# Performance work log

Hardware: AMD Instinct MI355X
Metric: run time of the kernel (lower is better)

## Reference

```python
import jax, jax.numpy as jnp
import numpy as np

MARGIN = 0.3
N = 8192
D = 128
NUM_CLASSES = 256

def setup_inputs() -> dict:
    key = jax.random.key(0)
    k1, k2 = jax.random.split(key)
    inputs = jax.random.normal(k1, (N, D), dtype=jnp.float32)
    targets = jax.random.randint(k2, (N,), 0, NUM_CLASSES, dtype=jnp.int64)
    return {"inputs": inputs, "targets": targets}

def reference(inputs, targets):
    n = inputs.shape[0]
    dt = inputs.dtype
    # pairwise euclidean distances: ||xi||^2 + ||xj||^2 - 2 xi.xj, clamped and sqrt'ed
    sq = jnp.sum(inputs * inputs, axis=1)                     # [n]
    d2 = sq[:, None] + sq[None, :] - 2.0 * (inputs @ inputs.T)
    dist = jnp.sqrt(jnp.clip(d2, 1e-12, None))                # [n, n]
    dsq = dist * dist                                         # squared dists used by the loss

    mask = targets[:, None] == targets[None, :]               # same-identity mask [n, n]

    # positives: torch code sorts and drops the smallest (the self-distance ~1e-6)
    pos_d = jnp.where(mask, dist, jnp.inf)
    min_idx = jnp.argmin(pos_d, axis=1)                       # index of dropped element per row
    excl = jnp.arange(n)[None, :] == min_idx[:, None]
    pos_valid = mask & ~excl                                  # remaining positives
    cnt_p = jnp.sum(pos_valid, axis=1).astype(dt)
    sigma_p = jnp.sum(jnp.where(pos_valid, dsq, 0.0), axis=1) / cnt_p
    max_p = jnp.max(jnp.where(pos_valid, dsq, -jnp.inf), axis=1)
    dist_ap = max_p / sigma_p + 0.5 * jnp.log(sigma_p)        # [n]

    # negatives: all different-identity entries
    neg = ~mask
    cnt_n = jnp.sum(neg, axis=1).astype(dt)
    sigma_n = jnp.sum(jnp.where(neg, dsq, 0.0), axis=1) / cnt_n
    min_n = jnp.min(jnp.where(neg, dsq, jnp.inf), axis=1)
    dist_an = min_n / sigma_n + 0.5 * jnp.log(sigma_n)        # [n]

    # MarginRankingLoss with y=1: mean(max(0, -(an - ap) + margin))
    loss = jnp.mean(jnp.maximum(dist_ap - dist_an + MARGIN, 0.0))
    return loss
```

## Files before the change

kernel.cpp:

```cpp
#include <hip/hip_runtime.h>
#include <math.h>


#define NROWS 8192
#define MARGIN_F 0.3f

typedef short bf16x8 __attribute__((ext_vector_type(8)));
typedef float f32x16 __attribute__((ext_vector_type(16)));
union U4B { uint4 u; bf16x8 h; };

__device__ __forceinline__ unsigned short f2bf(float x) {
    unsigned u = __float_as_uint(x);
    return (unsigned short)((u + 0x7fffu + ((u >> 16) & 1u)) >> 16);
}
__device__ __forceinline__ float bflo(unsigned u) { return __uint_as_float(u << 16); }
__device__ __forceinline__ float bfhi(unsigned u) { return __uint_as_float(u & 0xffff0000u); }

__global__ __launch_bounds__(256) void prep_kernel(const float* __restrict__ X,
                                                   const int* __restrict__ tgt,
                                                   float* __restrict__ sq,
                                                   float* __restrict__ upk,
                                                   unsigned int* __restrict__ Xbf,
                                                   unsigned int* __restrict__ Xbfn,
                                                   int* __restrict__ hist,
                                                   int* __restrict__ ccnt,
                                                   int* __restrict__ cstart,
                                                   float* __restrict__ S_class,
                                                   float* __restrict__ bsum,
                                                   float* __restrict__ rowsum) {
    __shared__ int h[256];
    __shared__ int csh[256];
    __shared__ int wsum[4];
    __shared__ float rsm[4][128];
    __shared__ float bs[4];
    int tid = threadIdx.x, w = tid >> 6, l = tid & 63;
    int bx = blockIdx.x;

    h[tid] = 0;
    __syncthreads();
    const int4* t4 = (const int4*)tgt;
    for (int i = tid; i < NROWS / 4; i += 256) {
        int4 v = t4[i];
        atomicAdd(&h[v.x], 1);
        atomicAdd(&h[v.y], 1);
        atomicAdd(&h[v.z], 1);
        atomicAdd(&h[v.w], 1);
    }
    __syncthreads();
    int hv = h[tid];
    int x = hv;
    #pragma unroll
    for (int d = 1; d < 64; d <<= 1) {
        int y = __shfl_up(x, d, 64);
        if ((tid & 63) >= d) x += y;
    }
    if ((tid & 63) == 63) wsum[tid >> 6] = x;
    __syncthreads();
    int off = 0;
    for (int i = 0; i < (tid >> 6); ++i) off += wsum[i];
    int excl = off + x - hv;
    csh[tid] = excl;
    if (bx == 0) {
        hist[tid] = hv;
        cstart[tid] = excl;
        if (tid == 255) cstart[256] = NROWS;
    }

    int row0 = bx * 32 + w * 8;
    unsigned h2s[8];
    float s8[8];
    int c8[8];
    float rsx = 0.0f, rsy = 0.0f, rs = 0.0f;
    #pragma unroll
    for (int i = 0; i < 8; ++i) {
        int r = row0 + i;
        float2 v = ((const float2*)X)[(size_t)r * 64 + l];
        unsigned hx = f2bf(v.x), hy = f2bf(v.y);
        h2s[i] = hx | (hy << 16);
        rsx += v.x; rsy += v.y;
        float s = v.x * v.x + v.y * v.y;
        for (int d = 32; d > 0; d >>= 1) s += __shfl_down(s, d, 64);
        if (l == 0) {
            c8[i] = tgt[r];
            s8[i] = s;
            rs += s;
        }
    }
    rsm[w][2 * l] = rsx;
    rsm[w][2 * l + 1] = rsy;
    if (l == 0) bs[w] = rs;
    __syncthreads();
    if (tid < 128)
        atomicAdd(&rowsum[tid], rsm[0][tid] + rsm[1][tid] + rsm[2][tid] + rsm[3][tid]);
    if (tid == 0) bsum[bx] = bs[0] + bs[1] + bs[2] + bs[3];

    #pragma unroll
    for (int i = 0; i < 8; ++i) {
        int pos = 0;
        if (l == 0) {
            int c = c8[i];
            pos = csh[c] + atomicAdd(&ccnt[c], 1);
            sq[pos] = s8[i];
            upk[pos] = __uint_as_float((__float_as_uint(0.5f * s8[i]) & 0xffffff00u) | (unsigned)c);
            atomicAdd(&S_class[c], s8[i]);
        }
        pos = __shfl(pos, 0, 64);
        int g = pos >> 5, rr = pos & 31;
        size_t idx = ((size_t)(g * 16 + (l >> 2)) * 32 + rr) * 4 + (l & 3);
        unsigned hh = h2s[i];
        Xbf[idx] = hh;
        Xbfn[idx] = hh ^ 0x80008000u;
    }
}

__global__ __launch_bounds__(256, 3) void dist_kernel(
        const unsigned short* __restrict__ Xbf, const unsigned short* __restrict__ Xbfn,
        const float* __restrict__ upk, const int* __restrict__ cstart,
        float4* __restrict__ partial, int ns_mask, int jb_shift, int tiles) {
    __shared__ float4 sm[64 * 4];
    const int tid = threadIdx.x;
    const int w = tid >> 6, l = tid & 63, hl = l >> 5, l31 = l & 31;
    const int bx = blockIdx.x;
    const int slice = bx & ns_mask;
    const int jb = bx >> jb_shift;
    const int col0 = jb * 64;
    const uint4* Xq = (const uint4*)Xbf;
    const uint4* Xqn = (const uint4*)Xbfn;

    bf16x8 Bf[2][8];
    #pragma unroll
    for (int ct = 0; ct < 2; ++ct) {
        const uint4* bp = Xq + (size_t)(jb * 2 + ct) * 512 + hl * 32 + l31;
        #pragma unroll
        for (int kk = 0; kk < 8; ++kk) {
            U4B tb; tb.u = bp[kk * 64];
            Bf[ct][kk] = tb.h;
        }
    }
    int tjt[2];
    tjt[0] = __float_as_int(upk[col0 + l31]) & 0xff;
    tjt[1] = __float_as_int(upk[col0 + 32 + l31]) & 0xff;
    const int c_first = __float_as_int(upk[col0]) & 0xff;
    const int c_last  = __float_as_int(upk[col0 + 63]) & 0xff;
    const int U0 = cstart[c_first];
    const int U1 = cstart[c_last + 1];

    float Ss[2] = {0.f, 0.f};
    float Mp[2] = {-INFINITY, -INFINITY};
    float Mn[2] = { INFINITY,  INFINITY};
    const int row_base = slice * tiles * 128;

    for (int t = 0; t < tiles; ++t) {
        const int i0 = row_base + t * 128;

        float ur[16];
        const float4* up = (const float4*)(upk + i0 + w * 32 + 4 * hl);
        #pragma unroll
        for (int g = 0; g < 4; ++g) {
            float4 u4 = up[g * 2];
            ur[g * 4 + 0] = u4.x; ur[g * 4 + 1] = u4.y;
            ur[g * 4 + 2] = u4.z; ur[g * 4 + 3] = u4.w;
        }

        f32x16 ainit;
        #pragma unroll
        for (int r = 0; r < 16; ++r) ainit[r] = ur[r];
        f32x16 acc[2];
        acc[0] = ainit;
        acc[1] = ainit;
        const uint4* ap = Xqn + ((size_t)(i0 >> 5) + w) * 512 + hl * 32 + l31;
        #pragma unroll
        for (int kk = 0; kk < 8; ++kk) {
            U4B a; a.u = ap[kk * 64];
            acc[0] = __builtin_amdgcn_mfma_f32_32x32x16_bf16(a.h, Bf[0][kk], acc[0], 0, 0, 0);
            acc[1] = __builtin_amdgcn_mfma_f32_32x32x16_bf16(a.h, Bf[1][kk], acc[1], 0, 0, 0);
        }

        if (i0 < U1 && i0 + 128 > U0) {
            #pragma unroll
            for (int ct = 0; ct < 2; ++ct) {
                const int tt = tjt[ct];
                #pragma unroll
                for (int r = 0; r < 16; ++r) {
                    float v = acc[ct][r];
                    bool same = ((__float_as_int(ur[r]) & 0xff) == tt);
                    float a = ur[r] - v;
                    Ss[ct] += same ? a : 0.0f;
                    Mp[ct] = fmaxf(Mp[ct], same ? v : -INFINITY);
                    Mn[ct] = same ? Mn[ct] : fminf(Mn[ct], v);
                }
            }
        } else {
            #pragma unroll
            for (int ct = 0; ct < 2; ++ct) {
                #pragma unroll
                for (int r = 0; r < 16; r += 2)
                    Mn[ct] = fminf(fminf(acc[ct][r], acc[ct][r + 1]), Mn[ct]);
            }
        }
    }

    #pragma unroll
    for (int ct = 0; ct < 2; ++ct) {
        Ss[ct] += __shfl_xor(Ss[ct], 32, 64);
        Mp[ct] = fmaxf(Mp[ct], __shfl_xor(Mp[ct], 32, 64));
        Mn[ct] = fminf(Mn[ct], __shfl_xor(Mn[ct], 32, 64));
    }
    if (l < 32) {
        #pragma unroll
        for (int ct = 0; ct < 2; ++ct)
            sm[(ct * 32 + l31) * 4 + w] = make_float4(Ss[ct], Mp[ct], Mn[ct], 0.0f);
    }
    __syncthreads();
    if (tid < 64) {
        float4 a = sm[tid * 4 + 0], b = sm[tid * 4 + 1];
        float4 c2 = sm[tid * 4 + 2], d = sm[tid * 4 + 3];
        float4 o;
        o.x = a.x + b.x + c2.x + d.x;
        o.y = fmaxf(fmaxf(a.y, b.y), fmaxf(c2.y, d.y));
        o.z = fminf(fminf(a.z, b.z), fminf(c2.z, d.z));
        o.w = 0.0f;
        partial[(size_t)slice * NROWS + col0 + tid] = o;
    }
}

__global__ __launch_bounds__(256) void combine_kernel(
        const float* __restrict__ sq, const float* __restrict__ upk,
        const unsigned int* __restrict__ Xbf,
        const int* __restrict__ hist, const float* __restrict__ S_class,
        const float* __restrict__ bsum, const float* __restrict__ rowsum,
        const float4* __restrict__ partial,
        float* __restrict__ blocksum, int* __restrict__ done,
        float* __restrict__ out, int ns) {
    __shared__ float red[4];
    __shared__ float hs[4];
    __shared__ float rsl[128];
    __shared__ int lastflag;
    int tid = threadIdx.x, l = tid & 63, w = tid >> 6;

    if (tid < 128) rsl[tid] = rowsum[tid];

    float b = bsum[tid];
    for (int d = 32; d > 0; d >>= 1) b += __shfl_down(b, d, 64);
    if (l == 0) red[w] = b;
    __syncthreads();
    float S_all = red[0] + red[1] + red[2] + red[3];

    int j = blockIdx.x * 256 + tid;
    float Ss = 0.f, Mp = -INFINITY, Mn = INFINITY;
    for (int s = 0; s < ns; ++s) {
        float4 p = partial[(size_t)s * NROWS + j];
        Ss += p.x;
        Mp = fmaxf(Mp, p.y); Mn = fminf(Mn, p.z);
    }

    float sa = 0.0f;
    {
        const uint4* Xq = (const uint4*)Xbf;
        int g = j >> 5, rr = j & 31;
        #pragma unroll
        for (int c16 = 0; c16 < 16; ++c16) {
            uint4 q = Xq[((size_t)(g * 16 + c16)) * 32 + rr];
            int k0 = c16 * 8;
            sa = fmaf(bflo(q.x), rsl[k0 + 0], sa);
            sa = fmaf(bfhi(q.x), rsl[k0 + 1], sa);
            sa = fmaf(bflo(q.y), rsl[k0 + 2], sa);
            sa = fmaf(bfhi(q.y), rsl[k0 + 3], sa);
            sa = fmaf(bflo(q.z), rsl[k0 + 4], sa);
            sa = fmaf(bfhi(q.z), rsl[k0 + 5], sa);
            sa = fmaf(bflo(q.w), rsl[k0 + 6], sa);
            sa = fmaf(bfhi(q.w), rsl[k0 + 7], sa);
        }
    }

    float sqj = sq[j];
    int c = __float_as_int(upk[j]) & 0xff;
    float cnt = (float)hist[c];
    float sumall = (float)NROWS * sqj + S_all - 2.0f * sa;
    float sump = cnt * sqj + S_class[c] - 2.0f * Ss;
    float sumn = sumall - sump;
    float sigp = sump / (cnt - 1.0f);
    float sign_ = sumn / ((float)NROWS - cnt);
    float ap = (sqj + 2.0f * Mp) / sigp + 0.5f * __logf(sigp);
    float an = (sqj + 2.0f * Mn) / sign_ + 0.5f * __logf(sign_);
    float h = fmaxf(ap - an + MARGIN_F, 0.0f);
    for (int d = 32; d > 0; d >>= 1) h += __shfl_down(h, d, 64);
    if (l == 0) hs[w] = h;
    __syncthreads();
    if (tid == 0) {
        float tot = hs[0] + hs[1] + hs[2] + hs[3];
        __hip_atomic_store(&blocksum[blockIdx.x], tot,
                           __ATOMIC_RELEASE, __HIP_MEMORY_SCOPE_AGENT);
        int prev = __hip_atomic_fetch_add(done, 1,
                                          __ATOMIC_ACQ_REL, __HIP_MEMORY_SCOPE_AGENT);
        lastflag = (prev == 31) ? 1 : 0;
    }
    __syncthreads();
    if (lastflag) {
        float s2 = 0.0f;
        if (tid < 32)
            s2 = __hip_atomic_load(&blocksum[tid],
                                   __ATOMIC_ACQUIRE, __HIP_MEMORY_SCOPE_AGENT);
        if (tid < 64) {
            for (int d = 32; d > 0; d >>= 1) s2 += __shfl_down(s2, d, 64);
            if (tid == 0) out[0] = s2 * (1.0f / NROWS);
        }
    }
}

extern "C" void kernel_launch(void* const* d_in, const int* in_sizes, int n_in,
                              void* d_out, int out_size, void* d_ws, size_t ws_size,
                              hipStream_t stream) {
    const float* X = (const float*)d_in[0];
    const int* tgt = (const int*)d_in[1];
    float* out = (float*)d_out;

    float* f = (float*)d_ws;
    int*   hist     = (int*)f;
    float* S_class  = f + 256;
    int*   ccnt     = (int*)(f + 512);
    float* rowsum   = f + 768;
    int*   done     = (int*)(f + 897);
    float* bsum     = f + 1024;
    float* blocksum = f + 1280;
    int*   cstart   = (int*)(f + 1536);
    float* sq       = f + 2048;
    float* upk      = f + 10240;
    unsigned int* Xbf  = (unsigned int*)(f + 18432);
    unsigned int* Xbfn = (unsigned int*)(f + 542720);
    float4* partial = (float4*)(f + 1067008);

    int ns = 8;
    while (ns > 2 && ws_size < ((size_t)1067008 + (size_t)ns * NROWS * 4) * sizeof(float))
        ns >>= 1;
    int shift = (ns == 8) ? 3 : (ns == 4) ? 2 : 1;
    int tiles = 64 / ns;

    hipMemsetAsync(d_ws, 0, 3600, stream);
    prep_kernel<<<256, 256, 0, stream>>>(X, tgt, sq, upk, Xbf, Xbfn,
                                         hist, ccnt, cstart, S_class, bsum, rowsum);
    dist_kernel<<<128 * ns, 256, 0, stream>>>((const unsigned short*)Xbf,
                                              (const unsigned short*)Xbfn,
                                              upk, cstart, partial,
                                              ns - 1, shift, tiles);
    combine_kernel<<<32, 256, 0, stream>>>(sq, upk, Xbf, hist, S_class, bsum,
                                           rowsum, partial, blocksum, done, out, ns);
}
```

Baseline: 113.2 us.

## Split histogram scan into single-block kernel, drop memset, raise dist occupancy

Moves the class histogram and prefix scan out of every prep block into one single-block kernel that also zeroes the accumulators, replacing the memset and the redundant per-block histogram work. Prep then takes positions from a global atomic offset per class. The dist kernel's launch bound rises from 3 to 4 waves per SIMD, and the per-tile ur register copy is reloaded only on the mixed-class path, which cuts register pressure. The cost is an extra serial single-block launch and possible register spills under the tighter bound.

```diff
diff --git a/kernel.cpp b/kernel.cpp
--- a/kernel.cpp
+++ b/kernel.cpp
@@ -15,6 +15,48 @@
 }
 __device__ __forceinline__ float bflo(unsigned u) { return __uint_as_float(u << 16); }
 __device__ __forceinline__ float bfhi(unsigned u) { return __uint_as_float(u & 0xffff0000u); }
+
+__global__ __launch_bounds__(256) void histscan_kernel(const int* __restrict__ tgt,
+                                                       int* __restrict__ hist,
+                                                       int* __restrict__ cstart,
+                                                       int* __restrict__ coffset,
+                                                       float* __restrict__ S_class,
+                                                       float* __restrict__ rowsum,
+                                                       int* __restrict__ done) {
+    __shared__ int h[256];
+    __shared__ int wsum[4];
+    int t = threadIdx.x;
+    h[t] = 0;
+    S_class[t] = 0.0f;
+    if (t < 128) rowsum[t] = 0.0f;
+    if (t == 0) *done = 0;
+    __syncthreads();
+    const int4* t4 = (const int4*)tgt;
+    for (int i = t; i < NROWS / 4; i += 256) {
+        int4 v = t4[i];
+        atomicAdd(&h[v.x], 1);
+        atomicAdd(&h[v.y], 1);
+        atomicAdd(&h[v.z], 1);
+        atomicAdd(&h[v.w], 1);
+    }
+    __syncthreads();
+    int hv = h[t];
+    hist[t] = hv;
+    int x = hv;
+    #pragma unroll
+    for (int d = 1; d < 64; d <<= 1) {
+        int y = __shfl_up(x, d, 64);
+        if ((t & 63) >= d) x += y;
+    }
+    if ((t & 63) == 63) wsum[t >> 6] = x;
+    __syncthreads();
+    int off = 0;
+    for (int i = 0; i < (t >> 6); ++i) off += wsum[i];
+    int excl = off + x - hv;
+    cstart[t] = excl;
+    coffset[t] = excl;
+    if (t == 255) cstart[256] = NROWS;
+}
 
 __global__ __launch_bounds__(256) void prep_kernel(const float* __restrict__ X,
                                                    const int* __restrict__ tgt,
@@ -22,55 +64,21 @@
                                                    float* __restrict__ upk,
                                                    unsigned int* __restrict__ Xbf,
                                                    unsigned int* __restrict__ Xbfn,
-                                                   int* __restrict__ hist,
-                                                   int* __restrict__ ccnt,
-                                                   int* __restrict__ cstart,
+                                                   int* __restrict__ coffset,
                                                    float* __restrict__ S_class,
                                                    float* __restrict__ bsum,
                                                    float* __restrict__ rowsum) {
-    __shared__ int h[256];
-    __shared__ int csh[256];
-    __shared__ int wsum[4];
     __shared__ float rsm[4][128];
     __shared__ float bs[4];
     int tid = threadIdx.x, w = tid >> 6, l = tid & 63;
     int bx = blockIdx.x;
-
-    h[tid] = 0;
-    __syncthreads();
-    const int4* t4 = (const int4*)tgt;
-    for (int i = tid; i < NROWS / 4; i += 256) {
-        int4 v = t4[i];
-        atomicAdd(&h[v.x], 1);
-        atomicAdd(&h[v.y], 1);
-        atomicAdd(&h[v.z], 1);
-        atomicAdd(&h[v.w], 1);
-    }
-    __syncthreads();
-    int hv = h[tid];
-    int x = hv;
-    #pragma unroll
-    for (int d = 1; d < 64; d <<= 1) {
-        int y = __shfl_up(x, d, 64);
-        if ((tid & 63) >= d) x += y;
-    }
-    if ((tid & 63) == 63) wsum[tid >> 6] = x;
-    __syncthreads();
-    int off = 0;
-    for (int i = 0; i < (tid >> 6); ++i) off += wsum[i];
-    int excl = off + x - hv;
-    csh[tid] = excl;
-    if (bx == 0) {
-        hist[tid] = hv;
-        cstart[tid] = excl;
-        if (tid == 255) cstart[256] = NROWS;
-    }
-
     int row0 = bx * 32 + w * 8;
+
     unsigned h2s[8];
     float s8[8];
     int c8[8];
     float rsx = 0.0f, rsy = 0.0f, rs = 0.0f;
+
     #pragma unroll
     for (int i = 0; i < 8; ++i) {
         int r = row0 + i;
@@ -99,7 +107,7 @@
         int pos = 0;
         if (l == 0) {
             int c = c8[i];
-            pos = csh[c] + atomicAdd(&ccnt[c], 1);
+            pos = atomicAdd(&coffset[c], 1);
             sq[pos] = s8[i];
             upk[pos] = __uint_as_float((__float_as_uint(0.5f * s8[i]) & 0xffffff00u) | (unsigned)c);
             atomicAdd(&S_class[c], s8[i]);
@@ -113,7 +121,7 @@
     }
 }
 
-__global__ __launch_bounds__(256, 3) void dist_kernel(
+__global__ __launch_bounds__(256, 4) void dist_kernel(
         const unsigned short* __restrict__ Xbf, const unsigned short* __restrict__ Xbfn,
         const float* __restrict__ upk, const int* __restrict__ cstart,
         float4* __restrict__ partial, int ns_mask, int jb_shift, int tiles) {
@@ -153,21 +161,16 @@
     for (int t = 0; t < tiles; ++t) {
         const int i0 = row_base + t * 128;
 
-        float ur[16];
+        f32x16 acc[2];
         const float4* up = (const float4*)(upk + i0 + w * 32 + 4 * hl);
         #pragma unroll
         for (int g = 0; g < 4; ++g) {
             float4 u4 = up[g * 2];
-            ur[g * 4 + 0] = u4.x; ur[g * 4 + 1] = u4.y;
-            ur[g * 4 + 2] = u4.z; ur[g * 4 + 3] = u4.w;
-        }
-
-        f32x16 ainit;
-        #pragma unroll
-        for (int r = 0; r < 16; ++r) ainit[r] = ur[r];
-        f32x16 acc[2];
-        acc[0] = ainit;
-        acc[1] = ainit;
+            acc[0][g * 4 + 0] = u4.x; acc[0][g * 4 + 1] = u4.y;
+            acc[0][g * 4 + 2] = u4.z; acc[0][g * 4 + 3] = u4.w;
+        }
+        acc[1] = acc[0];
+
         const uint4* ap = Xqn + ((size_t)(i0 >> 5) + w) * 512 + hl * 32 + l31;
         #pragma unroll
         for (int kk = 0; kk < 8; ++kk) {
@@ -177,6 +180,13 @@
         }
 
         if (i0 < U1 && i0 + 128 > U0) {
+            float ur[16];
+            #pragma unroll
+            for (int g = 0; g < 4; ++g) {
+                float4 u4 = up[g * 2];
+                ur[g * 4 + 0] = u4.x; ur[g * 4 + 1] = u4.y;
+                ur[g * 4 + 2] = u4.z; ur[g * 4 + 3] = u4.w;
+            }
             #pragma unroll
             for (int ct = 0; ct < 2; ++ct) {
                 const int tt = tjt[ct];
@@ -318,9 +328,9 @@
     float* f = (float*)d_ws;
     int*   hist     = (int*)f;
     float* S_class  = f + 256;
-    int*   ccnt     = (int*)(f + 512);
+    int*   coffset  = (int*)(f + 512);
     float* rowsum   = f + 768;
-    int*   done     = (int*)(f + 897);
+    int*   done     = (int*)(f + 896);
     float* bsum     = f + 1024;
     float* blocksum = f + 1280;
     int*   cstart   = (int*)(f + 1536);
@@ -336,9 +346,10 @@
     int shift = (ns == 8) ? 3 : (ns == 4) ? 2 : 1;
     int tiles = 64 / ns;
 
-    hipMemsetAsync(d_ws, 0, 3600, stream);
+    histscan_kernel<<<1, 256, 0, stream>>>(tgt, hist, cstart, coffset,
+                                           S_class, rowsum, done);
     prep_kernel<<<256, 256, 0, stream>>>(X, tgt, sq, upk, Xbf, Xbfn,
-                                         hist, ccnt, cstart, S_class, bsum, rowsum);
+                                         coffset, S_class, bsum, rowsum);
     dist_kernel<<<128 * ns, 256, 0, stream>>>((const unsigned short*)Xbf,
                                               (const unsigned short*)Xbfn,
                                               upk, cstart, partial,
```

New measurement: 123.8 us. 9.4% more time.
